# Kernel optimization log

Measured on AMD Instinct MI355X. Metric: run time of the kernel, lower is better.

Reference implementation:

```python
import jax, jax.numpy as jnp
import numpy as np

N_HEADS = 16


def setup_inputs() -> dict:
    key = jax.random.key(0)
    ks = jax.random.split(key, 9)
    B, S, D = 2, 2048, 1024
    s = 0.02
    return {
        "x": jax.random.normal(ks[0], (B, S, D), dtype=jnp.float32),
        "Wq": jax.random.normal(ks[1], (D, D), dtype=jnp.float32) * s,
        "bq": jax.random.normal(ks[2], (D,), dtype=jnp.float32) * s,
        "Wk": jax.random.normal(ks[3], (D, D), dtype=jnp.float32) * s,
        "bk": jax.random.normal(ks[4], (D,), dtype=jnp.float32) * s,
        "Wv": jax.random.normal(ks[5], (D, D), dtype=jnp.float32) * s,
        "bv": jax.random.normal(ks[6], (D,), dtype=jnp.float32) * s,
        "Wo": jax.random.normal(ks[7], (D, D), dtype=jnp.float32) * s,
        "bo": jax.random.normal(ks[8], (D,), dtype=jnp.float32) * s,
    }


def reference(x, Wq, bq, Wk, bk, Wv, bv, Wo, bo):
    B, S, D = x.shape
    H = N_HEADS
    hd = D // H
    # projections -> [B, H, S, hd]
    def heads(w, b):
        return (x @ w + b).reshape(B, S, H, hd).transpose(0, 2, 1, 3)
    Q, K, V = heads(Wq, bq), heads(Wk, bk), heads(Wv, bv)
    scores = jnp.einsum("bhqd,bhkd->bhqk", Q, K)
    causal = jnp.triu(jnp.ones((S, S), dtype=bool), k=1)  # True above diagonal
    scores = jnp.where(causal, -jnp.inf, scores)
    w = jax.nn.softmax(scores / jnp.sqrt(jnp.float32(hd)), axis=-1)
    ctx = jnp.einsum("bhqk,bhkd->bhqd", w, V).transpose(0, 2, 1, 3).reshape(B, S, D)
    return ctx @ Wo + bo
```

## Files before the change

### kernel.cpp

```cpp
#include <hip/hip_runtime.h>
#include <hip/hip_bf16.h>

typedef __attribute__((ext_vector_type(8))) short short8;
typedef __attribute__((ext_vector_type(4))) float floatx4;
typedef __attribute__((ext_vector_type(4))) int intx4;
typedef __attribute__((ext_vector_type(2))) int intx2;

#define D_MODEL 1024
#define SEQ     2048
#define NB      2
#define NH      16
#define HD      64
#define MROWS   4096
#define CZ      (0.125f * 1.44269504f)

__device__ __forceinline__ floatx4 mfma_bf16(short8 a, short8 b, floatx4 c) {
  return __builtin_amdgcn_mfma_f32_16x16x32_bf16(a, b, c, 0, 0, 0);
}

__device__ __forceinline__ void dma16(const __hip_bfloat16* g, __hip_bfloat16* l) {
  __builtin_amdgcn_global_load_lds(
      (const __attribute__((address_space(1))) void*)g,
      (__attribute__((address_space(3))) void*)l, 16, 0, 0);
}
#define WAIT_VM(n)  __asm__ __volatile__("s_waitcnt vmcnt(" #n ")" ::: "memory")
#define BARRIER()   __asm__ __volatile__("s_barrier" ::: "memory")
#define WAIT_LGKM() __asm__ __volatile__("s_waitcnt lgkmcnt(0)" ::: "memory")

__device__ __forceinline__ int pack2bf(float a, float b) {
  unsigned ua = __builtin_bit_cast(unsigned, a) + 0x8000u;
  unsigned ub = __builtin_bit_cast(unsigned, b) + 0x8000u;
  return (int)__builtin_amdgcn_perm(ub, ua, 0x07060302u);
}

__device__ __forceinline__ int cvtpk(float a, float b) {
  int r;
  __asm__("v_cvt_pk_bf16_f32 %0, %1, %2" : "=v"(r) : "v"(a), "v"(b));
  return r;
}

__global__ void prep_kernel(const float* __restrict__ x, __hip_bfloat16* __restrict__ xb,
                            const float* __restrict__ W0, const float* __restrict__ W1,
                            const float* __restrict__ W2, const float* __restrict__ W3,
                            __hip_bfloat16* __restrict__ T0, __hip_bfloat16* __restrict__ T1,
                            __hip_bfloat16* __restrict__ T2, __hip_bfloat16* __restrict__ T3) {
  const int z = blockIdx.z;
  if (z == 4) {
    const int tid = threadIdx.y * 32 + threadIdx.x;
    const int base = ((blockIdx.y * 32 + blockIdx.x) * 256 + tid) * 16;
#pragma unroll
    for (int c = 0; c < 4; c++) {
      float4 v = *(const float4*)(x + base + c * 4);
      __hip_bfloat16 tmp[4];
      tmp[0] = __float2bfloat16(v.x);
      tmp[1] = __float2bfloat16(v.y);
      tmp[2] = __float2bfloat16(v.z);
      tmp[3] = __float2bfloat16(v.w);
      *(ushort4*)(xb + base + c * 4) = *(ushort4*)tmp;
    }
    return;
  }
  const float* W = (z == 0) ? W0 : (z == 1) ? W1 : (z == 2) ? W2 : W3;
  __hip_bfloat16* Wt = (z == 0) ? T0 : (z == 1) ? T1 : (z == 2) ? T2 : T3;
  __shared__ float tile[32][33];
  int k0 = blockIdx.x * 32, n0 = blockIdx.y * 32;
  int tx = threadIdx.x, ty = threadIdx.y;
#pragma unroll
  for (int i = 0; i < 4; i++)
    tile[ty + 8 * i][tx] = W[(size_t)(k0 + ty + 8 * i) * D_MODEL + n0 + tx];
  __syncthreads();
#pragma unroll
  for (int i = 0; i < 4; i++)
    Wt[(size_t)(n0 + ty + 8 * i) * D_MODEL + k0 + tx] = __float2bfloat16(tile[tx][ty + 8 * i]);
}

template <int MODE>
__global__ __launch_bounds__(256) void gemm_kernel(
    const __hip_bfloat16* __restrict__ X,
    const __hip_bfloat16* __restrict__ Wt0, const __hip_bfloat16* __restrict__ Wt1,
    const __hip_bfloat16* __restrict__ Wt2,
    const float* __restrict__ b0, const float* __restrict__ b1, const float* __restrict__ b2,
    void* __restrict__ out0, void* __restrict__ out1, void* __restrict__ out2) {
  constexpr int MT = (MODE == 0) ? 128 : 64;
  constexpr int I = MT / 32;
  constexpr int NKT = D_MODEL / 32;
  constexpr int STAGE_BYTES = 3 * (MT * 32 + 128 * 32) * 2;
  constexpr int EPI_BYTES = 64 * 132 * 4;
  constexpr int SMEM_BYTES = (STAGE_BYTES > EPI_BYTES) ? STAGE_BYTES : EPI_BYTES;

  const int z = blockIdx.y;
  const __hip_bfloat16* Wt = (z == 0) ? Wt0 : (z == 1) ? Wt1 : Wt2;
  const float* bias = (z == 0) ? b0 : (z == 1) ? b1 : b2;
  void* outp = (z == 0) ? out0 : (z == 1) ? out1 : out2;
  const float scale = (MODE == 0 && z == 0) ? CZ : 1.f;

  __shared__ __attribute__((aligned(16))) char smem[SMEM_BYTES];
  __hip_bfloat16* As = (__hip_bfloat16*)smem;
  __hip_bfloat16* Bs = (__hip_bfloat16*)smem + 3 * MT * 32;
  float* Es = (float*)smem;

  const int n0 = blockIdx.x * 128;
  const int m0 = blockIdx.z * MT;
  const int t = threadIdx.x;
  const int lane = t & 63, w = t >> 6;
  const int wm = (w >> 1) * (MT / 2), wn = (w & 1) * 64;
  const int lr = lane & 15;
  const int lq = lane >> 4;

  const __hip_bfloat16* Xp = X + (size_t)m0 * D_MODEL;
  const __hip_bfloat16* Wp = Wt + (size_t)n0 * D_MODEL;

  const int lrow = lane >> 2;
  const int skg = (((lane & 3) ^ ((lane >> 3) & 3)) << 3);
  const int srowA = ((MT == 128) ? (w << 5) : (w << 4)) + lrow;
  const int sbA0 = (((MT == 128) ? (w << 5) : (w << 4)) << 5);
  const int sbA1 = sbA0 + (16 << 5);
  const int srowB = (w << 5) + lrow;
  const int sbB0 = ((w << 5) << 5);
  const int sbB1 = sbB0 + (16 << 5);

#define STAGE_G(kt_, buf_)                                                              \
  {                                                                                     \
    const int kn_ = (kt_) * 32;                                                         \
    __hip_bfloat16* A_ = As + (buf_) * (MT * 32);                                       \
    __hip_bfloat16* B_ = Bs + (buf_) * (128 * 32);                                      \
    dma16(Xp + (size_t)srowA * D_MODEL + kn_ + skg, A_ + sbA0);                         \
    if (MT == 128) dma16(Xp + (size_t)(srowA + 16) * D_MODEL + kn_ + skg, A_ + sbA1);   \
    dma16(Wp + (size_t)srowB * D_MODEL + kn_ + skg, B_ + sbB0);                         \
    dma16(Wp + (size_t)(srowB + 16) * D_MODEL + kn_ + skg, B_ + sbB1);                  \
  }

  floatx4 acc[I][4];
#pragma unroll
  for (int i = 0; i < I; i++)
#pragma unroll
    for (int j = 0; j < 4; j++) acc[i][j] = (floatx4){0.f, 0.f, 0.f, 0.f};

  STAGE_G(0, 0);
  STAGE_G(1, 1);

  const int rcol = ((lq ^ ((lr >> 1) & 3)) << 3);

  int cb = 0;
  for (int kt = 0; kt < NKT; kt++) {
    if (kt < NKT - 1) {
      if constexpr (MODE == 0) WAIT_VM(4);
      else                     WAIT_VM(3);
    } else {
      WAIT_VM(0);
    }
    BARRIER();
    if (kt + 2 < NKT) {
      const int nb = (cb == 0) ? 2 : cb - 1;
      STAGE_G(kt + 2, nb);
    }
    const __hip_bfloat16* Ac = As + cb * (MT * 32);
    const __hip_bfloat16* Bc = Bs + cb * (128 * 32);
    short8 af[I], bfr[4];
#pragma unroll
    for (int i = 0; i < I; i++) af[i] = *(const short8*)&Ac[(wm + i * 16 + lr) * 32 + rcol];
#pragma unroll
    for (int j = 0; j < 4; j++) bfr[j] = *(const short8*)&Bc[(wn + j * 16 + lr) * 32 + rcol];
#pragma unroll
    for (int i = 0; i < I; i++)
#pragma unroll
      for (int j = 0; j < 4; j++) acc[i][j] = mfma_bf16(af[i], bfr[j], acc[i][j]);
    cb = (cb == 2) ? 0 : cb + 1;
  }
#undef STAGE_G

  float bvj[4];
#pragma unroll
  for (int j = 0; j < 4; j++) bvj[j] = bias[n0 + wn + j * 16 + lr];

  if constexpr (MODE == 1) {
    BARRIER();
#pragma unroll
    for (int i = 0; i < I; i++) {
      const int rowb = wm + i * 16 + lq * 4;
#pragma unroll
      for (int j = 0; j < 4; j++)
#pragma unroll
        for (int r = 0; r < 4; r++)
          Es[(rowb + r) * 132 + wn + j * 16 + lr] = acc[i][j][r] + bvj[j];
    }
    WAIT_LGKM();
    BARRIER();
    const int L = t >> 2, nseg = (t & 3) * 32;
    float* op = (float*)outp + (size_t)(m0 + L) * D_MODEL + n0 + nseg;
    const float* src = &Es[L * 132 + nseg];
#pragma unroll
    for (int k = 0; k < 8; k++) *(float4*)(op + 4 * k) = *(const float4*)(src + 4 * k);
  } else if (z != 2) {
    for (int c = 0; c < 2; c++) {
      BARRIER();
#pragma unroll
      for (int i2 = 0; i2 < 2; i2++) {
        const int i = 2 * c + i2;
        const int rowb = (w >> 1) * 32 + i2 * 16 + lq * 4;
#pragma unroll
        for (int j = 0; j < 4; j++)
#pragma unroll
          for (int r = 0; r < 4; r++)
            Es[(rowb + r) * 132 + wn + j * 16 + lr] = (acc[i][j][r] + bvj[j]) * scale;
      }
      WAIT_LGKM();
      BARRIER();
      const int L = t >> 2, nseg = (t & 3) * 32;
      const int m = m0 + ((L >> 5) << 6) + (c << 5) + (L & 31);
      const int bb = m >> 11, s = m & 2047;
      const int nn = n0 + nseg;
      __hip_bfloat16* op = (__hip_bfloat16*)outp +
          (((size_t)(bb * NH + (nn >> 6)) * SEQ + s) * HD + (nn & 63));
      const float* src = &Es[L * 132 + nseg];
#pragma unroll
      for (int k = 0; k < 4; k++) {
        intx4 pk;
        pk[0] = pack2bf(src[8 * k + 0], src[8 * k + 1]);
        pk[1] = pack2bf(src[8 * k + 2], src[8 * k + 3]);
        pk[2] = pack2bf(src[8 * k + 4], src[8 * k + 5]);
        pk[3] = pack2bf(src[8 * k + 6], src[8 * k + 7]);
        *(intx4*)(op + 8 * k) = pk;
      }
    }
  } else {
    for (int c = 0; c < 2; c++) {
      BARRIER();
#pragma unroll
      for (int j2 = 0; j2 < 2; j2++) {
        const int j = 2 * c + j2;
        const int nl = ((w & 1) << 5) + (j2 << 4) + lr;
#pragma unroll
        for (int i = 0; i < I; i++) {
          const int moff = (w >> 1) * 64 + i * 16 + lq * 4;
          floatx4 v = acc[i][j];
          v[0] += bvj[j]; v[1] += bvj[j]; v[2] += bvj[j]; v[3] += bvj[j];
          *(floatx4*)&Es[nl * 132 + moff] = v;
        }
      }
      WAIT_LGKM();
      BARRIER();
      const int nl = t >> 2, mseg = (t & 3) * 32;
      const int n = n0 + ((nl >> 5) << 6) + (c << 5) + (nl & 31);
      const int s0 = m0 & 2047, bb = m0 >> 11;
      __hip_bfloat16* op = (__hip_bfloat16*)outp +
          (((size_t)(bb * NH + (n >> 6)) * HD + (n & 63)) * SEQ + s0 + mseg);
      const float* src = &Es[nl * 132 + mseg];
#pragma unroll
      for (int k = 0; k < 4; k++) {
        intx4 pk;
        pk[0] = pack2bf(src[8 * k + 0], src[8 * k + 1]);
        pk[1] = pack2bf(src[8 * k + 2], src[8 * k + 3]);
        pk[2] = pack2bf(src[8 * k + 4], src[8 * k + 5]);
        pk[3] = pack2bf(src[8 * k + 6], src[8 * k + 7]);
        *(intx4*)(op + 8 * k) = pk;
      }
    }
  }
}

__global__ __launch_bounds__(256, 4) void attn_kernel(
    const __hip_bfloat16* __restrict__ Q, const __hip_bfloat16* __restrict__ Kg,
    const __hip_bfloat16* __restrict__ Vt, __hip_bfloat16* __restrict__ ctx) {
  const int bh = blockIdx.x;
  const int b = bh >> 4, h = bh & 15;
  const int qt = 31 - blockIdx.y;
  const int t = threadIdx.x, lane = t & 63, w = t >> 6;
  const int lr = lane & 15, lq = lane >> 4;
  const int wr = w & 1, wb = w >> 1;

  __shared__ __attribute__((aligned(16))) __hip_bfloat16 Ks[2][64 * 64];
  __shared__ __attribute__((aligned(16))) __hip_bfloat16 VTs[2][64 * 64];

  const __hip_bfloat16* Qb = Q + (size_t)bh * SEQ * HD;
  const __hip_bfloat16* Kb = Kg + (size_t)bh * SEQ * HD;
  const __hip_bfloat16* Vb = Vt + (size_t)bh * HD * SEQ;

  const int qrow0 = qt * 64 + wr * 32;

  short8 qf[2][2];
#pragma unroll
  for (int rt = 0; rt < 2; rt++)
#pragma unroll
    for (int ks = 0; ks < 2; ks++)
      qf[rt][ks] = *(const short8*)(Qb + (size_t)(qrow0 + rt * 16 + lr) * HD + ks * 32 + lq * 8);

  const int srow = (w << 4) + (lane >> 3);
  const int sgl = lane & 7;
  const int sb0 = (w << 4) << 6;
  const int sb1 = ((w << 4) + 8) << 6;

#define STAGE(tb, nb)                                                                  \
  {                                                                                    \
    const int r0 = srow, r1 = srow + 8;                                                \
    dma16(Kb + ((size_t)((tb) + r0) << 6) + ((sgl ^ (r0 & 7)) << 3), &Ks[nb][sb0]);    \
    dma16(Kb + ((size_t)((tb) + r1) << 6) + ((sgl ^ (r1 & 7)) << 3), &Ks[nb][sb1]);    \
    dma16(Vb + (size_t)r0 * SEQ + (tb) + ((sgl ^ (r0 & 7)) << 3), &VTs[nb][sb0]);      \
    dma16(Vb + (size_t)r1 * SEQ + (tb) + ((sgl ^ (r1 & 7)) << 3), &VTs[nb][sb1]);      \
  }

  const int nkt = qt + 1;
  STAGE(0, 0);

  floatx4 o[2][4];
#pragma unroll
  for (int rt = 0; rt < 2; rt++)
#pragma unroll
    for (int dt = 0; dt < 4; dt++) o[rt][dt] = (floatx4){0.f, 0.f, 0.f, 0.f};
  floatx4 lsacc[2];
  lsacc[0] = (floatx4){0.f, 0.f, 0.f, 0.f};
  lsacc[1] = (floatx4){0.f, 0.f, 0.f, 0.f};

  short8 ones;
#pragma unroll
  for (int j = 0; j < 8; j++) ones[j] = (short)0x3F80;

  const int kfb0 = ((wb << 4) + lr) << 6;
  const int kg0 = ((lq ^ (lr & 7)) << 3);
  const int kg1 = (((4 + lq) ^ (lr & 7)) << 3);
  const int vga = (((wb * 2 + (lq >> 1)) ^ (lr & 7)) << 3) + ((lq & 1) << 2);
  const int vgb = (((4 + wb * 2 + (lq >> 1)) ^ (lr & 7)) << 3) + ((lq & 1) << 2);

  for (int kt = 0; kt < nkt; kt++) {
    WAIT_VM(0);
    BARRIER();
    if (kt + 1 < nkt) STAGE((kt + 1) << 6, (kt + 1) & 1);

    const int kw0 = (kt << 6) + (wb << 4);
    if (kw0 <= qrow0 + 31) {
      const __hip_bfloat16* Kc = Ks[kt & 1];
      const __hip_bfloat16* Vc = VTs[kt & 1];

      short8 kf[2][2];
#pragma unroll
      for (int nt = 0; nt < 2; nt++) {
        kf[0][nt] = *(const short8*)&Kc[(nt << 11) + kfb0 + kg0];
        kf[1][nt] = *(const short8*)&Kc[(nt << 11) + kfb0 + kg1];
      }
      floatx4 s[2][2];
#pragma unroll
      for (int rt = 0; rt < 2; rt++)
#pragma unroll
        for (int nt = 0; nt < 2; nt++) s[rt][nt] = (floatx4){0.f, 0.f, 0.f, 0.f};
#pragma unroll
      for (int ks = 0; ks < 2; ks++)
#pragma unroll
        for (int nt = 0; nt < 2; nt++) {
          s[0][nt] = mfma_bf16(kf[ks][nt], qf[0][ks], s[0][nt]);
          s[1][nt] = mfma_bf16(kf[ks][nt], qf[1][ks], s[1][nt]);
        }

      const bool need_mask = (kw0 + 47 > qrow0);
      short8 pf[2];
#pragma unroll
      for (int rt = 0; rt < 2; rt++) {
        const int q = qrow0 + rt * 16 + lr;
        intx4 pk;
#pragma unroll
        for (int nt = 0; nt < 2; nt++) {
          const int kbase = (kt << 6) + (nt << 5) + (wb << 4) + (lq << 2);
          float x0 = s[rt][nt][0], x1 = s[rt][nt][1], x2 = s[rt][nt][2], x3 = s[rt][nt][3];
          if (need_mask) {
            x0 = (kbase + 0 <= q) ? x0 : -1e30f;
            x1 = (kbase + 1 <= q) ? x1 : -1e30f;
            x2 = (kbase + 2 <= q) ? x2 : -1e30f;
            x3 = (kbase + 3 <= q) ? x3 : -1e30f;
          }
          const float p0 = __builtin_amdgcn_exp2f(x0);
          const float p1 = __builtin_amdgcn_exp2f(x1);
          const float p2 = __builtin_amdgcn_exp2f(x2);
          const float p3 = __builtin_amdgcn_exp2f(x3);
          pk[2 * nt + 0] = cvtpk(p0, p1);
          pk[2 * nt + 1] = cvtpk(p2, p3);
        }
        pf[rt] = __builtin_bit_cast(short8, pk);
      }

      lsacc[0] = mfma_bf16(ones, pf[0], lsacc[0]);
      lsacc[1] = mfma_bf16(ones, pf[1], lsacc[1]);

#pragma unroll
      for (int dt = 0; dt < 4; dt++) {
        const int rb = ((dt << 4) + lr) << 6;
        intx4 vi;
        *(intx2*)&vi = *(const intx2*)&Vc[rb + vga];
        *(((intx2*)&vi) + 1) = *(const intx2*)&Vc[rb + vgb];
        short8 vf = __builtin_bit_cast(short8, vi);
        o[0][dt] = mfma_bf16(vf, pf[0], o[0][dt]);
        o[1][dt] = mfma_bf16(vf, pf[1], o[1][dt]);
      }
    }
  }

  BARRIER();
  if (wb == 1) {
    float* d0 = (float*)&Ks[0][0];
    float* d1 = (float*)&Ks[1][0];
    float* dl = (float*)&VTs[0][0];
    const int base = (wr << 10) + (lane << 4);
#pragma unroll
    for (int dt = 0; dt < 4; dt++) *(floatx4*)&d0[base + (dt << 2)] = o[0][dt];
#pragma unroll
    for (int dt = 0; dt < 4; dt++) *(floatx4*)&d1[base + (dt << 2)] = o[1][dt];
    dl[(wr << 7) + (lane << 1)] = lsacc[0][0];
    dl[(wr << 7) + (lane << 1) + 1] = lsacc[1][0];
    WAIT_LGKM();
  }
  BARRIER();
  if (wb == 0) {
    const float* d0 = (const float*)&Ks[0][0];
    const float* d1 = (const float*)&Ks[1][0];
    const float* dl = (const float*)&VTs[0][0];
    const int base = (wr << 10) + (lane << 4);
#pragma unroll
    for (int dt = 0; dt < 4; dt++) {
      o[0][dt] += *(const floatx4*)&d0[base + (dt << 2)];
      o[1][dt] += *(const floatx4*)&d1[base + (dt << 2)];
    }
    float inv[2];
    inv[0] = 1.f / (lsacc[0][0] + dl[(wr << 7) + (lane << 1)]);
    inv[1] = 1.f / (lsacc[1][0] + dl[(wr << 7) + (lane << 1) + 1]);
#pragma unroll
    for (int rt = 0; rt < 2; rt++) {
      const int row = qrow0 + rt * 16 + lr;
      __hip_bfloat16* cp = ctx + (size_t)b * SEQ * D_MODEL + (size_t)row * D_MODEL + h * HD;
#pragma unroll
      for (int dt = 0; dt < 4; dt++) {
        ushort4 pk;
        __hip_bfloat16* pp = (__hip_bfloat16*)&pk;
#pragma unroll
        for (int r = 0; r < 4; r++) pp[r] = __float2bfloat16(o[rt][dt][r] * inv[rt]);
        *(ushort4*)(cp + (dt << 4) + (lq << 2)) = pk;
      }
    }
  }
#undef STAGE
}

extern "C" void kernel_launch(void* const* d_in, const int* in_sizes, int n_in,
                              void* d_out, int out_size, void* d_ws, size_t ws_size,
                              hipStream_t stream) {
  const float* x  = (const float*)d_in[0];
  const float* Wq = (const float*)d_in[1];
  const float* bq = (const float*)d_in[2];
  const float* Wk = (const float*)d_in[3];
  const float* bk = (const float*)d_in[4];
  const float* Wv = (const float*)d_in[5];
  const float* bv = (const float*)d_in[6];
  const float* Wo = (const float*)d_in[7];
  const float* bo = (const float*)d_in[8];

  char* ws = (char*)d_ws;
  const size_t MB = 1u << 20;
  __hip_bfloat16* xb  = (__hip_bfloat16*)(ws + 0 * MB);
  __hip_bfloat16* wtq = (__hip_bfloat16*)(ws + 8 * MB);
  __hip_bfloat16* wtk = (__hip_bfloat16*)(ws + 10 * MB);
  __hip_bfloat16* wtv = (__hip_bfloat16*)(ws + 12 * MB);
  __hip_bfloat16* wto = (__hip_bfloat16*)(ws + 14 * MB);
  __hip_bfloat16* qb  = (__hip_bfloat16*)(ws + 16 * MB);
  __hip_bfloat16* kb  = (__hip_bfloat16*)(ws + 24 * MB);
  __hip_bfloat16* vt  = (__hip_bfloat16*)(ws + 32 * MB);
  __hip_bfloat16* ctx = xb;

  prep_kernel<<<dim3(32, 32, 5), dim3(32, 8), 0, stream>>>(x, xb, Wq, Wk, Wv, Wo,
                                                           wtq, wtk, wtv, wto);
  gemm_kernel<0><<<dim3(8, 3, 32), 256, 0, stream>>>(xb, wtq, wtk, wtv, bq, bk, bv,
                                                     (void*)qb, (void*)kb, (void*)vt);
  attn_kernel<<<dim3(32, 32), 256, 0, stream>>>(qb, kb, vt, ctx);
  gemm_kernel<1><<<dim3(8, 1, 64), 256, 0, stream>>>(ctx, wto, wto, wto, bo, bo, bo,
                                                     d_out, d_out, d_out);
}
```

Baseline: 185.0 us.

## Double attention query tile to 128 rows per block for K/V reuse

Each attention block now handles 128 query rows instead of 64, with each warp holding 4 row-tiles, so every K/V tile staged in shared memory is reused across twice as many queries. V fragments are loaded once per key tile and shared across the row tiles. The grid is halved, launch bounds drop to 2 blocks per SM to allow more registers, and the cross-warp reduction of partial outputs runs in two passes. This costs fewer resident blocks, coarser causal load balance, and higher register pressure.

```diff
diff --git a/kernel.cpp b/kernel.cpp
--- a/kernel.cpp
+++ b/kernel.cpp
@@ -259,12 +259,12 @@
   }
 }
 
-__global__ __launch_bounds__(256, 4) void attn_kernel(
+__global__ __launch_bounds__(256, 2) void attn_kernel(
     const __hip_bfloat16* __restrict__ Q, const __hip_bfloat16* __restrict__ Kg,
     const __hip_bfloat16* __restrict__ Vt, __hip_bfloat16* __restrict__ ctx) {
   const int bh = blockIdx.x;
   const int b = bh >> 4, h = bh & 15;
-  const int qt = 31 - blockIdx.y;
+  const int qt = 15 - blockIdx.y;
   const int t = threadIdx.x, lane = t & 63, w = t >> 6;
   const int lr = lane & 15, lq = lane >> 4;
   const int wr = w & 1, wb = w >> 1;
@@ -276,11 +276,11 @@
   const __hip_bfloat16* Kb = Kg + (size_t)bh * SEQ * HD;
   const __hip_bfloat16* Vb = Vt + (size_t)bh * HD * SEQ;
 
-  const int qrow0 = qt * 64 + wr * 32;
-
-  short8 qf[2][2];
-#pragma unroll
-  for (int rt = 0; rt < 2; rt++)
+  const int qrow0 = qt * 128 + wr * 64;
+
+  short8 qf[4][2];
+#pragma unroll
+  for (int rt = 0; rt < 4; rt++)
 #pragma unroll
     for (int ks = 0; ks < 2; ks++)
       qf[rt][ks] = *(const short8*)(Qb + (size_t)(qrow0 + rt * 16 + lr) * HD + ks * 32 + lq * 8);
@@ -299,17 +299,17 @@
     dma16(Vb + (size_t)r1 * SEQ + (tb) + ((sgl ^ (r1 & 7)) << 3), &VTs[nb][sb1]);      \
   }
 
-  const int nkt = qt + 1;
+  const int nkt = 2 * qt + 2;
   STAGE(0, 0);
 
-  floatx4 o[2][4];
-#pragma unroll
-  for (int rt = 0; rt < 2; rt++)
+  floatx4 o[4][4];
+#pragma unroll
+  for (int rt = 0; rt < 4; rt++)
 #pragma unroll
     for (int dt = 0; dt < 4; dt++) o[rt][dt] = (floatx4){0.f, 0.f, 0.f, 0.f};
-  floatx4 lsacc[2];
-  lsacc[0] = (floatx4){0.f, 0.f, 0.f, 0.f};
-  lsacc[1] = (floatx4){0.f, 0.f, 0.f, 0.f};
+  floatx4 lsacc[4];
+#pragma unroll
+  for (int rt = 0; rt < 4; rt++) lsacc[rt] = (floatx4){0.f, 0.f, 0.f, 0.f};
 
   short8 ones;
 #pragma unroll
@@ -327,7 +327,7 @@
     if (kt + 1 < nkt) STAGE((kt + 1) << 6, (kt + 1) & 1);
 
     const int kw0 = (kt << 6) + (wb << 4);
-    if (kw0 <= qrow0 + 31) {
+    if (kw0 <= qrow0 + 63) {
       const __hip_bfloat16* Kc = Ks[kt & 1];
       const __hip_bfloat16* Vc = VTs[kt & 1];
 
@@ -337,30 +337,34 @@
         kf[0][nt] = *(const short8*)&Kc[(nt << 11) + kfb0 + kg0];
         kf[1][nt] = *(const short8*)&Kc[(nt << 11) + kfb0 + kg1];
       }
-      floatx4 s[2][2];
-#pragma unroll
-      for (int rt = 0; rt < 2; rt++)
-#pragma unroll
-        for (int nt = 0; nt < 2; nt++) s[rt][nt] = (floatx4){0.f, 0.f, 0.f, 0.f};
-#pragma unroll
-      for (int ks = 0; ks < 2; ks++)
-#pragma unroll
-        for (int nt = 0; nt < 2; nt++) {
-          s[0][nt] = mfma_bf16(kf[ks][nt], qf[0][ks], s[0][nt]);
-          s[1][nt] = mfma_bf16(kf[ks][nt], qf[1][ks], s[1][nt]);
-        }
-
-      const bool need_mask = (kw0 + 47 > qrow0);
-      short8 pf[2];
-#pragma unroll
-      for (int rt = 0; rt < 2; rt++) {
+      short8 vfr[4];
+#pragma unroll
+      for (int dt = 0; dt < 4; dt++) {
+        const int rb = ((dt << 4) + lr) << 6;
+        intx4 vi;
+        *(intx2*)&vi = *(const intx2*)&Vc[rb + vga];
+        *(((intx2*)&vi) + 1) = *(const intx2*)&Vc[rb + vgb];
+        vfr[dt] = __builtin_bit_cast(short8, vi);
+      }
+
+#pragma unroll
+      for (int rt = 0; rt < 4; rt++) {
+        floatx4 s0 = (floatx4){0.f, 0.f, 0.f, 0.f};
+        floatx4 s1 = (floatx4){0.f, 0.f, 0.f, 0.f};
+        s0 = mfma_bf16(kf[0][0], qf[rt][0], s0);
+        s0 = mfma_bf16(kf[1][0], qf[rt][1], s0);
+        s1 = mfma_bf16(kf[0][1], qf[rt][0], s1);
+        s1 = mfma_bf16(kf[1][1], qf[rt][1], s1);
+
+        const bool nm = (kw0 + 47 > qrow0 + rt * 16);
         const int q = qrow0 + rt * 16 + lr;
         intx4 pk;
 #pragma unroll
         for (int nt = 0; nt < 2; nt++) {
+          const floatx4 sv = nt ? s1 : s0;
           const int kbase = (kt << 6) + (nt << 5) + (wb << 4) + (lq << 2);
-          float x0 = s[rt][nt][0], x1 = s[rt][nt][1], x2 = s[rt][nt][2], x3 = s[rt][nt][3];
-          if (need_mask) {
+          float x0 = sv[0], x1 = sv[1], x2 = sv[2], x3 = sv[3];
+          if (nm) {
             x0 = (kbase + 0 <= q) ? x0 : -1e30f;
             x1 = (kbase + 1 <= q) ? x1 : -1e30f;
             x2 = (kbase + 2 <= q) ? x2 : -1e30f;
@@ -373,64 +377,58 @@
           pk[2 * nt + 0] = cvtpk(p0, p1);
           pk[2 * nt + 1] = cvtpk(p2, p3);
         }
-        pf[rt] = __builtin_bit_cast(short8, pk);
-      }
-
-      lsacc[0] = mfma_bf16(ones, pf[0], lsacc[0]);
-      lsacc[1] = mfma_bf16(ones, pf[1], lsacc[1]);
-
+        const short8 pf = __builtin_bit_cast(short8, pk);
+
+        lsacc[rt] = mfma_bf16(ones, pf, lsacc[rt]);
+#pragma unroll
+        for (int dt = 0; dt < 4; dt++)
+          o[rt][dt] = mfma_bf16(vfr[dt], pf, o[rt][dt]);
+      }
+    }
+  }
+
+  for (int c = 0; c < 2; c++) {
+    BARRIER();
+    if (wb == 1) {
+      float* d0 = (float*)&Ks[0][0];
+      float* d1 = (float*)&Ks[1][0];
+      float* dl = (float*)&VTs[0][0];
+      const int base = (wr << 10) + (lane << 4);
+#pragma unroll
+      for (int dt = 0; dt < 4; dt++) *(floatx4*)&d0[base + (dt << 2)] = o[2 * c + 0][dt];
+#pragma unroll
+      for (int dt = 0; dt < 4; dt++) *(floatx4*)&d1[base + (dt << 2)] = o[2 * c + 1][dt];
+      dl[(wr << 7) + (lane << 1)] = lsacc[2 * c + 0][0];
+      dl[(wr << 7) + (lane << 1) + 1] = lsacc[2 * c + 1][0];
+      WAIT_LGKM();
+    }
+    BARRIER();
+    if (wb == 0) {
+      const float* d0 = (const float*)&Ks[0][0];
+      const float* d1 = (const float*)&Ks[1][0];
+      const float* dl = (const float*)&VTs[0][0];
+      const int base = (wr << 10) + (lane << 4);
+      floatx4 om[2][4];
 #pragma unroll
       for (int dt = 0; dt < 4; dt++) {
-        const int rb = ((dt << 4) + lr) << 6;
-        intx4 vi;
-        *(intx2*)&vi = *(const intx2*)&Vc[rb + vga];
-        *(((intx2*)&vi) + 1) = *(const intx2*)&Vc[rb + vgb];
-        short8 vf = __builtin_bit_cast(short8, vi);
-        o[0][dt] = mfma_bf16(vf, pf[0], o[0][dt]);
-        o[1][dt] = mfma_bf16(vf, pf[1], o[1][dt]);
-      }
-    }
-  }
-
-  BARRIER();
-  if (wb == 1) {
-    float* d0 = (float*)&Ks[0][0];
-    float* d1 = (float*)&Ks[1][0];
-    float* dl = (float*)&VTs[0][0];
-    const int base = (wr << 10) + (lane << 4);
-#pragma unroll
-    for (int dt = 0; dt < 4; dt++) *(floatx4*)&d0[base + (dt << 2)] = o[0][dt];
-#pragma unroll
-    for (int dt = 0; dt < 4; dt++) *(floatx4*)&d1[base + (dt << 2)] = o[1][dt];
-    dl[(wr << 7) + (lane << 1)] = lsacc[0][0];
-    dl[(wr << 7) + (lane << 1) + 1] = lsacc[1][0];
-    WAIT_LGKM();
-  }
-  BARRIER();
-  if (wb == 0) {
-    const float* d0 = (const float*)&Ks[0][0];
-    const float* d1 = (const float*)&Ks[1][0];
-    const float* dl = (const float*)&VTs[0][0];
-    const int base = (wr << 10) + (lane << 4);
-#pragma unroll
-    for (int dt = 0; dt < 4; dt++) {
-      o[0][dt] += *(const floatx4*)&d0[base + (dt << 2)];
-      o[1][dt] += *(const floatx4*)&d1[base + (dt << 2)];
-    }
-    float inv[2];
-    inv[0] = 1.f / (lsacc[0][0] + dl[(wr << 7) + (lane << 1)]);
-    inv[1] = 1.f / (lsacc[1][0] + dl[(wr << 7) + (lane << 1) + 1]);
-#pragma unroll
-    for (int rt = 0; rt < 2; rt++) {
-      const int row = qrow0 + rt * 16 + lr;
-      __hip_bfloat16* cp = ctx + (size_t)b * SEQ * D_MODEL + (size_t)row * D_MODEL + h * HD;
-#pragma unroll
-      for (int dt = 0; dt < 4; dt++) {
-        ushort4 pk;
-        __hip_bfloat16* pp = (__hip_bfloat16*)&pk;
-#pragma unroll
-        for (int r = 0; r < 4; r++) pp[r] = __float2bfloat16(o[rt][dt][r] * inv[rt]);
-        *(ushort4*)(cp + (dt << 4) + (lq << 2)) = pk;
+        om[0][dt] = o[2 * c + 0][dt] + *(const floatx4*)&d0[base + (dt << 2)];
+        om[1][dt] = o[2 * c + 1][dt] + *(const floatx4*)&d1[base + (dt << 2)];
+      }
+      float inv[2];
+      inv[0] = 1.f / (lsacc[2 * c + 0][0] + dl[(wr << 7) + (lane << 1)]);
+      inv[1] = 1.f / (lsacc[2 * c + 1][0] + dl[(wr << 7) + (lane << 1) + 1]);
+#pragma unroll
+      for (int j = 0; j < 2; j++) {
+        const int row = qrow0 + (2 * c + j) * 16 + lr;
+        __hip_bfloat16* cp = ctx + (size_t)b * SEQ * D_MODEL + (size_t)row * D_MODEL + h * HD;
+#pragma unroll
+        for (int dt = 0; dt < 4; dt++) {
+          ushort4 pk;
+          __hip_bfloat16* pp = (__hip_bfloat16*)&pk;
+#pragma unroll
+          for (int r = 0; r < 4; r++) pp[r] = __float2bfloat16(om[j][dt][r] * inv[j]);
+          *(ushort4*)(cp + (dt << 4) + (lq << 2)) = pk;
+        }
       }
     }
   }
@@ -466,7 +464,7 @@
                                                            wtq, wtk, wtv, wto);
   gemm_kernel<0><<<dim3(8, 3, 32), 256, 0, stream>>>(xb, wtq, wtk, wtv, bq, bk, bv,
                                                      (void*)qb, (void*)kb, (void*)vt);
-  attn_kernel<<<dim3(32, 32), 256, 0, stream>>>(qb, kb, vt, ctx);
+  attn_kernel<<<dim3(32, 16), 256, 0, stream>>>(qb, kb, vt, ctx);
   gemm_kernel<1><<<dim3(8, 1, 64), 256, 0, stream>>>(ctx, wto, wto, wto, bo, bo, bo,
                                                      d_out, d_out, d_out);
 }
```

Result: slower. 192.5 us (+4.1%).

## Load K and V fragments directly from global memory, dropping LDS staging

Applied to the files above, without the earlier changes.

The attention inner loop no longer double-buffers K and V^T tiles into shared memory through async global-to-LDS DMA with barriers. Each wave now reads its MFMA operand fragments straight from global memory (relying on cache) and the per-tile barrier and vmcnt wait are removed. The per-wave skip of fully masked key subtiles is also dropped, so masked tiles are still computed. The cost is global latency exposed inside the loop with no prefetch, plus redundant global traffic, because the two waves sharing a key half each fetch the same K/V data.

```diff
diff --git a/kernel.cpp b/kernel.cpp
--- a/kernel.cpp
+++ b/kernel.cpp
@@ -270,7 +270,7 @@
   const int wr = w & 1, wb = w >> 1;
 
   __shared__ __attribute__((aligned(16))) __hip_bfloat16 Ks[2][64 * 64];
-  __shared__ __attribute__((aligned(16))) __hip_bfloat16 VTs[2][64 * 64];
+  __shared__ __attribute__((aligned(16))) __hip_bfloat16 VTs[1][64 * 64];
 
   const __hip_bfloat16* Qb = Q + (size_t)bh * SEQ * HD;
   const __hip_bfloat16* Kb = Kg + (size_t)bh * SEQ * HD;
@@ -285,22 +285,7 @@
     for (int ks = 0; ks < 2; ks++)
       qf[rt][ks] = *(const short8*)(Qb + (size_t)(qrow0 + rt * 16 + lr) * HD + ks * 32 + lq * 8);
 
-  const int srow = (w << 4) + (lane >> 3);
-  const int sgl = lane & 7;
-  const int sb0 = (w << 4) << 6;
-  const int sb1 = ((w << 4) + 8) << 6;
-
-#define STAGE(tb, nb)                                                                  \
-  {                                                                                    \
-    const int r0 = srow, r1 = srow + 8;                                                \
-    dma16(Kb + ((size_t)((tb) + r0) << 6) + ((sgl ^ (r0 & 7)) << 3), &Ks[nb][sb0]);    \
-    dma16(Kb + ((size_t)((tb) + r1) << 6) + ((sgl ^ (r1 & 7)) << 3), &Ks[nb][sb1]);    \
-    dma16(Vb + (size_t)r0 * SEQ + (tb) + ((sgl ^ (r0 & 7)) << 3), &VTs[nb][sb0]);      \
-    dma16(Vb + (size_t)r1 * SEQ + (tb) + ((sgl ^ (r1 & 7)) << 3), &VTs[nb][sb1]);      \
-  }
-
   const int nkt = qt + 1;
-  STAGE(0, 0);
 
   floatx4 o[2][4];
 #pragma unroll
@@ -315,80 +300,76 @@
 #pragma unroll
   for (int j = 0; j < 8; j++) ones[j] = (short)0x3F80;
 
-  const int kfb0 = ((wb << 4) + lr) << 6;
-  const int kg0 = ((lq ^ (lr & 7)) << 3);
-  const int kg1 = (((4 + lq) ^ (lr & 7)) << 3);
-  const int vga = (((wb * 2 + (lq >> 1)) ^ (lr & 7)) << 3) + ((lq & 1) << 2);
-  const int vgb = (((4 + wb * 2 + (lq >> 1)) ^ (lr & 7)) << 3) + ((lq & 1) << 2);
+  const __hip_bfloat16* Kfb = Kb + (size_t)((wb << 4) + lr) * HD;
+  const __hip_bfloat16* Vfb = Vb + (size_t)lr * SEQ + (wb << 4) + (lq << 2);
 
   for (int kt = 0; kt < nkt; kt++) {
-    WAIT_VM(0);
-    BARRIER();
-    if (kt + 1 < nkt) STAGE((kt + 1) << 6, (kt + 1) & 1);
-
     const int kw0 = (kt << 6) + (wb << 4);
-    if (kw0 <= qrow0 + 31) {
-      const __hip_bfloat16* Kc = Ks[kt & 1];
-      const __hip_bfloat16* Vc = VTs[kt & 1];
-
-      short8 kf[2][2];
+
+    short8 kf[2][2];
+    const __hip_bfloat16* Kt = Kfb + ((size_t)kt << 12);
+#pragma unroll
+    for (int nt = 0; nt < 2; nt++) {
+      kf[0][nt] = *(const short8*)(Kt + (nt << 11) + (lq << 3));
+      kf[1][nt] = *(const short8*)(Kt + (nt << 11) + 32 + (lq << 3));
+    }
+    short8 vfr[4];
+    const __hip_bfloat16* Vtp = Vfb + (kt << 6);
+#pragma unroll
+    for (int dt = 0; dt < 4; dt++) {
+      const __hip_bfloat16* vp = Vtp + (size_t)(dt << 4) * SEQ;
+      intx4 vi;
+      *(intx2*)&vi = *(const intx2*)vp;
+      *(((intx2*)&vi) + 1) = *(const intx2*)(vp + 32);
+      vfr[dt] = __builtin_bit_cast(short8, vi);
+    }
+
+    floatx4 s[2][2];
+#pragma unroll
+    for (int rt = 0; rt < 2; rt++)
+#pragma unroll
+      for (int nt = 0; nt < 2; nt++) s[rt][nt] = (floatx4){0.f, 0.f, 0.f, 0.f};
+#pragma unroll
+    for (int ks = 0; ks < 2; ks++)
 #pragma unroll
       for (int nt = 0; nt < 2; nt++) {
-        kf[0][nt] = *(const short8*)&Kc[(nt << 11) + kfb0 + kg0];
-        kf[1][nt] = *(const short8*)&Kc[(nt << 11) + kfb0 + kg1];
-      }
-      floatx4 s[2][2];
-#pragma unroll
-      for (int rt = 0; rt < 2; rt++)
-#pragma unroll
-        for (int nt = 0; nt < 2; nt++) s[rt][nt] = (floatx4){0.f, 0.f, 0.f, 0.f};
-#pragma unroll
-      for (int ks = 0; ks < 2; ks++)
-#pragma unroll
-        for (int nt = 0; nt < 2; nt++) {
-          s[0][nt] = mfma_bf16(kf[ks][nt], qf[0][ks], s[0][nt]);
-          s[1][nt] = mfma_bf16(kf[ks][nt], qf[1][ks], s[1][nt]);
+        s[0][nt] = mfma_bf16(kf[ks][nt], qf[0][ks], s[0][nt]);
+        s[1][nt] = mfma_bf16(kf[ks][nt], qf[1][ks], s[1][nt]);
+      }
+
+    const bool need_mask = (kw0 + 47 > qrow0);
+    short8 pf[2];
+#pragma unroll
+    for (int rt = 0; rt < 2; rt++) {
+      const int q = qrow0 + rt * 16 + lr;
+      intx4 pk;
+#pragma unroll
+      for (int nt = 0; nt < 2; nt++) {
+        const int kbase = (kt << 6) + (nt << 5) + (wb << 4) + (lq << 2);
+        float x0 = s[rt][nt][0], x1 = s[rt][nt][1], x2 = s[rt][nt][2], x3 = s[rt][nt][3];
+        if (need_mask) {
+          x0 = (kbase + 0 <= q) ? x0 : -1e30f;
+          x1 = (kbase + 1 <= q) ? x1 : -1e30f;
+          x2 = (kbase + 2 <= q) ? x2 : -1e30f;
+          x3 = (kbase + 3 <= q) ? x3 : -1e30f;
         }
-
-      const bool need_mask = (kw0 + 47 > qrow0);
-      short8 pf[2];
-#pragma unroll
-      for (int rt = 0; rt < 2; rt++) {
-        const int q = qrow0 + rt * 16 + lr;
-        intx4 pk;
-#pragma unroll
-        for (int nt = 0; nt < 2; nt++) {
-          const int kbase = (kt << 6) + (nt << 5) + (wb << 4) + (lq << 2);
-          float x0 = s[rt][nt][0], x1 = s[rt][nt][1], x2 = s[rt][nt][2], x3 = s[rt][nt][3];
-          if (need_mask) {
-            x0 = (kbase + 0 <= q) ? x0 : -1e30f;
-            x1 = (kbase + 1 <= q) ? x1 : -1e30f;
-            x2 = (kbase + 2 <= q) ? x2 : -1e30f;
-            x3 = (kbase + 3 <= q) ? x3 : -1e30f;
-          }
-          const float p0 = __builtin_amdgcn_exp2f(x0);
-          const float p1 = __builtin_amdgcn_exp2f(x1);
-          const float p2 = __builtin_amdgcn_exp2f(x2);
-          const float p3 = __builtin_amdgcn_exp2f(x3);
-          pk[2 * nt + 0] = cvtpk(p0, p1);
-          pk[2 * nt + 1] = cvtpk(p2, p3);
-        }
-        pf[rt] = __builtin_bit_cast(short8, pk);
-      }
-
-      lsacc[0] = mfma_bf16(ones, pf[0], lsacc[0]);
-      lsacc[1] = mfma_bf16(ones, pf[1], lsacc[1]);
-
-#pragma unroll
-      for (int dt = 0; dt < 4; dt++) {
-        const int rb = ((dt << 4) + lr) << 6;
-        intx4 vi;
-        *(intx2*)&vi = *(const intx2*)&Vc[rb + vga];
-        *(((intx2*)&vi) + 1) = *(const intx2*)&Vc[rb + vgb];
-        short8 vf = __builtin_bit_cast(short8, vi);
-        o[0][dt] = mfma_bf16(vf, pf[0], o[0][dt]);
-        o[1][dt] = mfma_bf16(vf, pf[1], o[1][dt]);
-      }
+        const float p0 = __builtin_amdgcn_exp2f(x0);
+        const float p1 = __builtin_amdgcn_exp2f(x1);
+        const float p2 = __builtin_amdgcn_exp2f(x2);
+        const float p3 = __builtin_amdgcn_exp2f(x3);
+        pk[2 * nt + 0] = cvtpk(p0, p1);
+        pk[2 * nt + 1] = cvtpk(p2, p3);
+      }
+      pf[rt] = __builtin_bit_cast(short8, pk);
+    }
+
+    lsacc[0] = mfma_bf16(ones, pf[0], lsacc[0]);
+    lsacc[1] = mfma_bf16(ones, pf[1], lsacc[1]);
+
+#pragma unroll
+    for (int dt = 0; dt < 4; dt++) {
+      o[0][dt] = mfma_bf16(vfr[dt], pf[0], o[0][dt]);
+      o[1][dt] = mfma_bf16(vfr[dt], pf[1], o[1][dt]);
     }
   }
 
@@ -434,7 +415,6 @@
       }
     }
   }
-#undef STAGE
 }
 
 extern "C" void kernel_launch(void* const* d_in, const int* in_sizes, int n_in,
```

Measured after the change: 260.0 us. 40.6% more time.
